# Performance work log

Measured on AMD Instinct MI355X. Metric: run time of the kernel, lower is better.

## Reference

```python
import jax, jax.numpy as jnp
import numpy as np

D_MODEL = 1024
N_HEADS = 16
D_HEAD = D_MODEL // N_HEADS


def setup_inputs() -> dict:
    key = jax.random.key(0)
    ks = jax.random.split(key, 5)
    scale = 1.0 / np.sqrt(D_MODEL)
    return {
        "x": jax.random.normal(ks[0], (2, 2048, D_MODEL), dtype=jnp.float32),
        "W_q": jax.random.normal(ks[1], (D_MODEL, D_MODEL), dtype=jnp.float32) * scale,
        "W_k": jax.random.normal(ks[2], (D_MODEL, D_MODEL), dtype=jnp.float32) * scale,
        "W_v": jax.random.normal(ks[3], (D_MODEL, D_MODEL), dtype=jnp.float32) * scale,
        "W_o": jax.random.normal(ks[4], (D_MODEL, D_MODEL), dtype=jnp.float32) * scale,
    }


def reference(x, W_q, W_k, W_v, W_o):
    B, S, _ = x.shape
    # nn.Linear computes x @ W.T; weights stored [out, in]
    def proj(W):
        y = jnp.einsum("bsd,ed->bse", x, W)
        return y.reshape(B, S, N_HEADS, D_HEAD).transpose(0, 2, 1, 3)  # [B,H,S,Dh]

    q, k, v = proj(W_q), proj(W_k), proj(W_v)
    scores = jnp.einsum("bhqd,bhkd->bhqk", q, k) / jnp.sqrt(jnp.float32(D_HEAD))
    causal = jnp.triu(jnp.ones((S, S), dtype=bool), k=1)
    scores = jnp.where(causal, -jnp.inf, scores)
    attn = jax.nn.softmax(scores, axis=-1)
    out = jnp.einsum("bhqk,bhkd->bhqd", attn, v)  # [B,H,S,Dh]
    out = out.transpose(0, 2, 1, 3).reshape(B, S, D_MODEL)
    return jnp.einsum("bsd,ed->bse", out, W_o)
```

## Files before the change

kernel.cpp:

```cpp
#include <hip/hip_runtime.h>


#define DMODEL 1024
#define NHEADS 16
#define DHEAD  64
#define SEQ    2048
#define BATCH  2
#define MROWS  (BATCH * SEQ)

typedef __bf16 bf16x8 __attribute__((ext_vector_type(8)));
typedef __bf16 bf16x4 __attribute__((ext_vector_type(4)));
typedef float  f32x4  __attribute__((ext_vector_type(4)));

__device__ __forceinline__ f32x4 mfma16(bf16x8 a, bf16x8 b, f32x4 c) {
    return __builtin_amdgcn_mfma_f32_16x16x32_bf16(a, b, c, 0, 0, 0);
}

__device__ __forceinline__ bf16x8 ld8(const float* p) {
    const f32x4 a0 = *(const f32x4*)p;
    const f32x4 a1 = *(const f32x4*)(p + 4);
    bf16x8 v;
    v[0] = (__bf16)a0[0]; v[1] = (__bf16)a0[1];
    v[2] = (__bf16)a0[2]; v[3] = (__bf16)a0[3];
    v[4] = (__bf16)a1[0]; v[5] = (__bf16)a1[1];
    v[6] = (__bf16)a1[2]; v[7] = (__bf16)a1[3];
    return v;
}

__device__ __forceinline__ void gll16(const __bf16* g, __bf16* l) {
    __builtin_amdgcn_global_load_lds(
        (const __attribute__((address_space(1))) void*)g,
        (__attribute__((address_space(3))) void*)l,
        16, 0, 0);
}

__global__ __launch_bounds__(256) void cvt_kernel(const float* __restrict__ x,
                                                  const float* __restrict__ Wq,
                                                  const float* __restrict__ Wk,
                                                  const float* __restrict__ Wv,
                                                  const float* __restrict__ Wo,
                                                  __bf16* __restrict__ xb,
                                                  __bf16* __restrict__ wcat) {
    const int y = blockIdx.y;
    const float* src;
    __bf16* dst;
    int nchunks;
    if (y == 0) { src = x; dst = xb; nchunks = (MROWS * DMODEL) / 8; }
    else {
        src = (y == 1) ? Wq : (y == 2) ? Wk : (y == 3) ? Wv : Wo;
        dst = wcat + (size_t)(y - 1) * DMODEL * DMODEL;
        nchunks = (DMODEL * DMODEL) / 8;
    }
    const int c = blockIdx.x * 256 + threadIdx.x;
    if (c < nchunks) *(bf16x8*)(dst + (size_t)c * 8) = ld8(src + (size_t)c * 8);
}

template <typename TC>
__device__ __forceinline__ void gemm_bb_body(const __bf16* __restrict__ A,
                                             const __bf16* __restrict__ W,
                                             TC* __restrict__ C,
                                             int m0, int n0, float scale) {
    constexpr int K = DMODEL;
    __shared__ __align__(16) __bf16 As[128][32];
    __shared__ __align__(16) __bf16 Bs[128][32];

    const int tid  = threadIdx.x;
    const int lane = tid & 63;
    const int wave = tid >> 6;
    const int quad = lane >> 4;
    const int l16  = lane & 15;
    const int wm   = wave & 1;
    const int wn   = wave >> 1;

    const int srow = lane >> 2;
    const int scol = (lane & 3) * 8;

    const __bf16* a0p = A + (size_t)(m0 + wave * 16 + srow) * K + scol;
    const __bf16* a1p = A + (size_t)(m0 + 64 + wave * 16 + srow) * K + scol;
    const __bf16* b0p = W + (size_t)(n0 + wave * 16 + srow) * K + scol;
    const __bf16* b1p = W + (size_t)(n0 + 64 + wave * 16 + srow) * K + scol;

    f32x4 acc[4][4] = {};

    for (int k0 = 0; k0 < K; k0 += 32) {
        __syncthreads();
        gll16(a0p + k0, &As[wave * 16][0]);
        gll16(a1p + k0, &As[64 + wave * 16][0]);
        gll16(b0p + k0, &Bs[wave * 16][0]);
        gll16(b1p + k0, &Bs[64 + wave * 16][0]);
        __syncthreads();

        bf16x8 af[4], bfr[4];
#pragma unroll
        for (int i = 0; i < 4; ++i) {
            af[i]  = *(const bf16x8*)(&As[wm * 64 + i * 16 + l16][quad * 8]);
            bfr[i] = *(const bf16x8*)(&Bs[wn * 64 + i * 16 + l16][quad * 8]);
        }
#pragma unroll
        for (int mi = 0; mi < 4; ++mi)
#pragma unroll
            for (int ni = 0; ni < 4; ++ni)
                acc[mi][ni] = mfma16(af[mi], bfr[ni], acc[mi][ni]);
    }

#pragma unroll
    for (int mi = 0; mi < 4; ++mi)
#pragma unroll
        for (int ni = 0; ni < 4; ++ni)
#pragma unroll
            for (int r = 0; r < 4; ++r) {
                int row = m0 + wm * 64 + mi * 16 + quad * 4 + r;
                int col = n0 + wn * 64 + ni * 16 + l16;
                C[(size_t)row * DMODEL + col] = (TC)(acc[mi][ni][r] * scale);
            }
}

#define QSCALE 0.1803368801111204f

__global__ __launch_bounds__(256) void qkv_kernel(const __bf16* __restrict__ X,
                                                  const __bf16* __restrict__ wcat,
                                                  __bf16* __restrict__ QKV) {
    const __bf16* W = wcat + (size_t)blockIdx.z * DMODEL * DMODEL;
    __bf16*       Y = QKV + (size_t)blockIdx.z * MROWS * DMODEL;
    const float scale = (blockIdx.z == 0) ? QSCALE : 1.0f;
    gemm_bb_body<__bf16>(X, W, Y, blockIdx.y * 128, blockIdx.x * 128, scale);
}

__global__ __launch_bounds__(256) void out_gemm_kernel(const __bf16* __restrict__ A,
                                                       const __bf16* __restrict__ W,
                                                       float* __restrict__ C) {
    gemm_bb_body<float>(A, W, C, blockIdx.y * 128, blockIdx.x * 128, 1.0f);
}

__global__ __launch_bounds__(128) void attn_kernel(const __bf16* __restrict__ Q,
                                                   const __bf16* __restrict__ Kg,
                                                   const __bf16* __restrict__ Vg,
                                                   __bf16* __restrict__ O) {
    const int bh = blockIdx.x;
    const int qt = 63 - blockIdx.y;
    const int b = bh >> 4, h = bh & 15;
    const size_t base = (size_t)b * SEQ * DMODEL + (size_t)h * DHEAD;

    const int tid  = threadIdx.x;
    const int lane = tid & 63;
    const int wave = tid >> 6;
    const int quad = lane >> 4;
    const int l16  = lane & 15;

    __shared__ __align__(16) __bf16 Ks[32][80];
    __shared__ __align__(16) __bf16 Vt[64][40];
    __shared__ __align__(16) __bf16 Ps[2][16][40];

    const int ldr = tid >> 2;
    const int c0  = (tid & 3) * 16;
    const int vcol = (((ldr >> 3) ^ (c0 >> 4)) << 3) | (ldr & 7);

    const int qrow = qt * 32 + wave * 16 + l16;

    const bf16x8 qf0 = *(const bf16x8*)(Q + base + (size_t)qrow * DMODEL + quad * 8);
    const bf16x8 qf1 = *(const bf16x8*)(Q + base + (size_t)qrow * DMODEL + 32 + quad * 8);

    f32x4 oacc[4] = {};
    float m_i = -1e30f, l_i = 0.f;

    const __bf16* kp = Kg + base + (size_t)ldr * DMODEL + c0;
    const __bf16* vp = Vg + base + (size_t)ldr * DMODEL + c0;
    bf16x8 pk0 = *(const bf16x8*)(kp);
    bf16x8 pk1 = *(const bf16x8*)(kp + 8);
    bf16x8 pv0 = *(const bf16x8*)(vp);
    bf16x8 pv1 = *(const bf16x8*)(vp + 8);

    for (int kt = 0; kt <= qt; ++kt) {
        *(bf16x8*)(&Ks[ldr][c0])     = pk0;
        *(bf16x8*)(&Ks[ldr][c0 + 8]) = pk1;
#pragma unroll
        for (int i = 0; i < 8; ++i) {
            Vt[c0 + i][vcol]     = pv0[i];
            Vt[c0 + 8 + i][vcol] = pv1[i];
        }
        __syncthreads();

        if (kt < qt) {
            const __bf16* kp2 = Kg + base + (size_t)((kt + 1) * 32 + ldr) * DMODEL + c0;
            const __bf16* vp2 = Vg + base + (size_t)((kt + 1) * 32 + ldr) * DMODEL + c0;
            pk0 = *(const bf16x8*)(kp2);
            pk1 = *(const bf16x8*)(kp2 + 8);
            pv0 = *(const bf16x8*)(vp2);
            pv1 = *(const bf16x8*)(vp2 + 8);
        }

        const int k0 = kt * 32;
        const bool diag = (kt == qt);

        const bf16x8 kf00 = *(const bf16x8*)(&Ks[l16][quad * 8]);
        const bf16x8 kf01 = *(const bf16x8*)(&Ks[l16][32 + quad * 8]);
        const bf16x8 kf10 = *(const bf16x8*)(&Ks[16 + l16][quad * 8]);
        const bf16x8 kf11 = *(const bf16x8*)(&Ks[16 + l16][32 + quad * 8]);
        f32x4 s0 = {}, s1 = {};
        s0 = mfma16(kf00, qf0, s0); s0 = mfma16(kf01, qf1, s0);
        s1 = mfma16(kf10, qf0, s1); s1 = mfma16(kf11, qf1, s1);

        float mx;
        bool ok[2][4];
        if (!diag) {
            float m0 = s0[0];
#pragma unroll
            for (int r = 1; r < 4; ++r) m0 = fmaxf(m0, s0[r]);
#pragma unroll
            for (int r = 0; r < 4; ++r) m0 = fmaxf(m0, s1[r]);
            mx = m0;
        } else {
            mx = -1e30f;
#pragma unroll
            for (int hh = 0; hh < 2; ++hh)
#pragma unroll
                for (int r = 0; r < 4; ++r) {
                    const int kk = k0 + hh * 16 + quad * 4 + r;
                    ok[hh][r] = (kk <= qrow);
                    const float v = hh ? s1[r] : s0[r];
                    mx = fmaxf(mx, ok[hh][r] ? v : -1e30f);
                }
        }
        mx = fmaxf(mx, __shfl_xor(mx, 16));
        mx = fmaxf(mx, __shfl_xor(mx, 32));
        const float mnew  = fmaxf(m_i, mx);
        const float alpha = exp2f(m_i - mnew);
        m_i = mnew;

        float p[2][4];
        float rs = 0.f;
        if (!diag) {
#pragma unroll
            for (int hh = 0; hh < 2; ++hh)
#pragma unroll
                for (int r = 0; r < 4; ++r) {
                    p[hh][r] = exp2f((hh ? s1[r] : s0[r]) - mnew);
                    rs += p[hh][r];
                }
        } else {
#pragma unroll
            for (int hh = 0; hh < 2; ++hh)
#pragma unroll
                for (int r = 0; r < 4; ++r) {
                    p[hh][r] = ok[hh][r] ? exp2f((hh ? s1[r] : s0[r]) - mnew) : 0.f;
                    rs += p[hh][r];
                }
        }
        rs += __shfl_xor(rs, 16);
        rs += __shfl_xor(rs, 32);
        l_i = l_i * alpha + rs;

        bf16x4 w0, w1;
#pragma unroll
        for (int r = 0; r < 4; ++r) { w0[r] = (__bf16)p[0][r]; w1[r] = (__bf16)p[1][r]; }
        *(bf16x4*)(&Ps[wave][l16][quad * 4])      = w0;
        *(bf16x4*)(&Ps[wave][l16][16 + quad * 4]) = w1;

        const bf16x8 pf = *(const bf16x8*)(&Ps[wave][l16][quad * 8]);
#pragma unroll
        for (int f = 0; f < 4; ++f) {
            const bf16x8 vf = *(const bf16x8*)(&Vt[f * 16 + l16][(quad ^ f) * 8]);
            oacc[f] = mfma16(vf, pf, oacc[f] * alpha);
        }
        __syncthreads();
    }

    const float inv = (l_i > 0.f) ? (1.f / l_i) : 0.f;
#pragma unroll
    for (int f = 0; f < 4; ++f) {
        bf16x4 o;
#pragma unroll
        for (int r = 0; r < 4; ++r) o[r] = (__bf16)(oacc[f][r] * inv);
        *(bf16x4*)(O + base + (size_t)qrow * DMODEL + f * 16 + quad * 4) = o;
    }
}

extern "C" void kernel_launch(void* const* d_in, const int* in_sizes, int n_in,
                              void* d_out, int out_size, void* d_ws, size_t ws_size,
                              hipStream_t stream) {
    const float* x  = (const float*)d_in[0];
    const float* Wq = (const float*)d_in[1];
    const float* Wk = (const float*)d_in[2];
    const float* Wv = (const float*)d_in[3];
    const float* Wo = (const float*)d_in[4];
    float* out = (float*)d_out;

    const size_t tm = (size_t)MROWS * DMODEL;
    const size_t tw = (size_t)DMODEL * DMODEL;
    __bf16* QKV  = (__bf16*)d_ws;
    __bf16* xb   = QKV + 3 * tm;
    __bf16* wcat = xb + tm;
    __bf16* Q = QKV;
    __bf16* K = QKV + tm;
    __bf16* V = QKV + 2 * tm;

    dim3 gc(2048, 5);
    cvt_kernel<<<gc, 256, 0, stream>>>(x, Wq, Wk, Wv, Wo, xb, wcat);

    dim3 g1(DMODEL / 128, MROWS / 128, 3);
    qkv_kernel<<<g1, 256, 0, stream>>>(xb, wcat, QKV);

    dim3 g2(BATCH * NHEADS, SEQ / 32);
    attn_kernel<<<g2, 128, 0, stream>>>(Q, K, V, Q);

    dim3 g3(DMODEL / 128, MROWS / 128);
    out_gemm_kernel<<<g3, 256, 0, stream>>>(Q, wcat + 3 * tw, out);
}
```

Baseline: 203.2 us.

## Write V transposed from QKV GEMM and load attention tiles via direct-to-LDS loads

The QKV GEMM now writes V in a transposed [head_dim, tokens] layout, and its K step doubles to 64 with an XOR-swizzled LDS layout. The attention kernel stages K and V^T tiles with direct global-to-LDS loads instead of register prefetch plus a scalar transpose scatter into shared memory. This removes the per-element V transpose in attention and the padded LDS arrays. In exchange it drops the register prefetch overlap and the trailing barrier, and the transposed V store from the GEMM is narrow and strided.

Result: slower. 217.5 us (+7.0%).

```diff
diff --git a/kernel.cpp b/kernel.cpp
--- a/kernel.cpp
+++ b/kernel.cpp
@@ -59,10 +59,12 @@
 __device__ __forceinline__ void gemm_bb_body(const __bf16* __restrict__ A,
                                              const __bf16* __restrict__ W,
                                              TC* __restrict__ C,
-                                             int m0, int n0, float scale) {
+                                             __bf16* __restrict__ VT,
+                                             bool vt, int m0, int n0,
+                                             float scale) {
     constexpr int K = DMODEL;
-    __shared__ __align__(16) __bf16 As[128][32];
-    __shared__ __align__(16) __bf16 Bs[128][32];
+    __shared__ __align__(16) __bf16 As[128][64];
+    __shared__ __align__(16) __bf16 Bs[128][64];
 
     const int tid  = threadIdx.x;
     const int lane = tid & 63;
@@ -72,69 +74,89 @@
     const int wm   = wave & 1;
     const int wn   = wave >> 1;
 
-    const int srow = lane >> 2;
-    const int scol = (lane & 3) * 8;
-
-    const __bf16* a0p = A + (size_t)(m0 + wave * 16 + srow) * K + scol;
-    const __bf16* a1p = A + (size_t)(m0 + 64 + wave * 16 + srow) * K + scol;
-    const __bf16* b0p = W + (size_t)(n0 + wave * 16 + srow) * K + scol;
-    const __bf16* b1p = W + (size_t)(n0 + 64 + wave * 16 + srow) * K + scol;
+    const int sr = lane >> 3;
+    const int sc = ((lane & 7) ^ sr) * 8;
 
     f32x4 acc[4][4] = {};
 
-    for (int k0 = 0; k0 < K; k0 += 32) {
+    for (int k0 = 0; k0 < K; k0 += 64) {
         __syncthreads();
-        gll16(a0p + k0, &As[wave * 16][0]);
-        gll16(a1p + k0, &As[64 + wave * 16][0]);
-        gll16(b0p + k0, &Bs[wave * 16][0]);
-        gll16(b1p + k0, &Bs[64 + wave * 16][0]);
+#pragma unroll
+        for (int s = 0; s < 4; ++s) {
+            const int row = s * 32 + wave * 8 + sr;
+            gll16(A + (size_t)(m0 + row) * K + k0 + sc, &As[s * 32 + wave * 8][0]);
+            gll16(W + (size_t)(n0 + row) * K + k0 + sc, &Bs[s * 32 + wave * 8][0]);
+        }
         __syncthreads();
 
-        bf16x8 af[4], bfr[4];
-#pragma unroll
-        for (int i = 0; i < 4; ++i) {
-            af[i]  = *(const bf16x8*)(&As[wm * 64 + i * 16 + l16][quad * 8]);
-            bfr[i] = *(const bf16x8*)(&Bs[wn * 64 + i * 16 + l16][quad * 8]);
-        }
+#pragma unroll
+        for (int h = 0; h < 2; ++h) {
+            bf16x8 af[4], bfr[4];
+#pragma unroll
+            for (int i = 0; i < 4; ++i) {
+                const int gr = ((h * 4 + quad) ^ (l16 & 7)) * 8;
+                af[i]  = *(const bf16x8*)(&As[wm * 64 + i * 16 + l16][gr]);
+                bfr[i] = *(const bf16x8*)(&Bs[wn * 64 + i * 16 + l16][gr]);
+            }
+#pragma unroll
+            for (int mi = 0; mi < 4; ++mi)
+#pragma unroll
+                for (int ni = 0; ni < 4; ++ni)
+                    acc[mi][ni] = mfma16(af[mi], bfr[ni], acc[mi][ni]);
+        }
+    }
+
+    if (!vt) {
 #pragma unroll
         for (int mi = 0; mi < 4; ++mi)
 #pragma unroll
             for (int ni = 0; ni < 4; ++ni)
-                acc[mi][ni] = mfma16(af[mi], bfr[ni], acc[mi][ni]);
-    }
-
-#pragma unroll
-    for (int mi = 0; mi < 4; ++mi)
-#pragma unroll
-        for (int ni = 0; ni < 4; ++ni)
-#pragma unroll
-            for (int r = 0; r < 4; ++r) {
-                int row = m0 + wm * 64 + mi * 16 + quad * 4 + r;
-                int col = n0 + wn * 64 + ni * 16 + l16;
-                C[(size_t)row * DMODEL + col] = (TC)(acc[mi][ni][r] * scale);
+#pragma unroll
+                for (int r = 0; r < 4; ++r) {
+                    int row = m0 + wm * 64 + mi * 16 + quad * 4 + r;
+                    int col = n0 + wn * 64 + ni * 16 + l16;
+                    C[(size_t)row * DMODEL + col] = (TC)(acc[mi][ni][r] * scale);
+                }
+    } else {
+#pragma unroll
+        for (int mi = 0; mi < 4; ++mi)
+#pragma unroll
+            for (int ni = 0; ni < 4; ++ni) {
+                const int m  = m0 + wm * 64 + mi * 16 + quad * 4;
+                const int hd = n0 + wn * 64 + ni * 16 + l16;
+                bf16x4 v4;
+#pragma unroll
+                for (int r = 0; r < 4; ++r) v4[r] = (__bf16)acc[mi][ni][r];
+                *(bf16x4*)(VT + (size_t)hd * MROWS + m) = v4;
             }
+    }
 }
 
 #define QSCALE 0.1803368801111204f
 
 __global__ __launch_bounds__(256) void qkv_kernel(const __bf16* __restrict__ X,
                                                   const __bf16* __restrict__ wcat,
-                                                  __bf16* __restrict__ QKV) {
-    const __bf16* W = wcat + (size_t)blockIdx.z * DMODEL * DMODEL;
-    __bf16*       Y = QKV + (size_t)blockIdx.z * MROWS * DMODEL;
-    const float scale = (blockIdx.z == 0) ? QSCALE : 1.0f;
-    gemm_bb_body<__bf16>(X, W, Y, blockIdx.y * 128, blockIdx.x * 128, scale);
+                                                  __bf16* __restrict__ Q,
+                                                  __bf16* __restrict__ K,
+                                                  __bf16* __restrict__ VT) {
+    const int z = blockIdx.z;
+    const __bf16* W = wcat + (size_t)z * DMODEL * DMODEL;
+    __bf16* Y = (z == 0) ? Q : K;
+    const float scale = (z == 0) ? QSCALE : 1.0f;
+    gemm_bb_body<__bf16>(X, W, Y, VT, z == 2,
+                         blockIdx.y * 128, blockIdx.x * 128, scale);
 }
 
 __global__ __launch_bounds__(256) void out_gemm_kernel(const __bf16* __restrict__ A,
                                                        const __bf16* __restrict__ W,
                                                        float* __restrict__ C) {
-    gemm_bb_body<float>(A, W, C, blockIdx.y * 128, blockIdx.x * 128, 1.0f);
+    gemm_bb_body<float>(A, W, C, nullptr, false,
+                        blockIdx.y * 128, blockIdx.x * 128, 1.0f);
 }
 
 __global__ __launch_bounds__(128) void attn_kernel(const __bf16* __restrict__ Q,
                                                    const __bf16* __restrict__ Kg,
-                                                   const __bf16* __restrict__ Vg,
+                                                   const __bf16* __restrict__ VTg,
                                                    __bf16* __restrict__ O) {
     const int bh = blockIdx.x;
     const int qt = 63 - blockIdx.y;
@@ -147,13 +169,14 @@
     const int quad = lane >> 4;
     const int l16  = lane & 15;
 
-    __shared__ __align__(16) __bf16 Ks[32][80];
-    __shared__ __align__(16) __bf16 Vt[64][40];
+    __shared__ __align__(16) __bf16 Ks[32][64];
+    __shared__ __align__(16) __bf16 Vs[64][32];
     __shared__ __align__(16) __bf16 Ps[2][16][40];
 
-    const int ldr = tid >> 2;
-    const int c0  = (tid & 3) * 16;
-    const int vcol = (((ldr >> 3) ^ (c0 >> 4)) << 3) | (ldr & 7);
+    const int ksr = lane >> 3;
+    const int ksc = ((lane & 7) ^ ksr) * 8;
+    const int vsr = lane >> 2;
+    const int vsc = ((lane & 3) ^ ((lane >> 3) & 3)) * 8;
 
     const int qrow = qt * 32 + wave * 16 + l16;
 
@@ -163,39 +186,27 @@
     f32x4 oacc[4] = {};
     float m_i = -1e30f, l_i = 0.f;
 
-    const __bf16* kp = Kg + base + (size_t)ldr * DMODEL + c0;
-    const __bf16* vp = Vg + base + (size_t)ldr * DMODEL + c0;
-    bf16x8 pk0 = *(const bf16x8*)(kp);
-    bf16x8 pk1 = *(const bf16x8*)(kp + 8);
-    bf16x8 pv0 = *(const bf16x8*)(vp);
-    bf16x8 pv1 = *(const bf16x8*)(vp + 8);
-
     for (int kt = 0; kt <= qt; ++kt) {
-        *(bf16x8*)(&Ks[ldr][c0])     = pk0;
-        *(bf16x8*)(&Ks[ldr][c0 + 8]) = pk1;
-#pragma unroll
-        for (int i = 0; i < 8; ++i) {
-            Vt[c0 + i][vcol]     = pv0[i];
-            Vt[c0 + 8 + i][vcol] = pv1[i];
-        }
+        const int k0 = kt * 32;
         __syncthreads();
-
-        if (kt < qt) {
-            const __bf16* kp2 = Kg + base + (size_t)((kt + 1) * 32 + ldr) * DMODEL + c0;
-            const __bf16* vp2 = Vg + base + (size_t)((kt + 1) * 32 + ldr) * DMODEL + c0;
-            pk0 = *(const bf16x8*)(kp2);
-            pk1 = *(const bf16x8*)(kp2 + 8);
-            pv0 = *(const bf16x8*)(vp2);
-            pv1 = *(const bf16x8*)(vp2 + 8);
-        }
-
-        const int k0 = kt * 32;
+#pragma unroll
+        for (int j = 0; j < 2; ++j) {
+            gll16(Kg + base + (size_t)(k0 + wave * 16 + j * 8 + ksr) * DMODEL + ksc,
+                  &Ks[wave * 16 + j * 8][0]);
+            gll16(VTg + (size_t)(h * 64 + j * 32 + wave * 16 + vsr) * MROWS
+                      + (size_t)b * SEQ + k0 + vsc,
+                  &Vs[j * 32 + wave * 16][0]);
+        }
+        __syncthreads();
+
         const bool diag = (kt == qt);
 
-        const bf16x8 kf00 = *(const bf16x8*)(&Ks[l16][quad * 8]);
-        const bf16x8 kf01 = *(const bf16x8*)(&Ks[l16][32 + quad * 8]);
-        const bf16x8 kf10 = *(const bf16x8*)(&Ks[16 + l16][quad * 8]);
-        const bf16x8 kf11 = *(const bf16x8*)(&Ks[16 + l16][32 + quad * 8]);
+        const int g0 = ((quad ^ (l16 & 7))) * 8;
+        const int g1 = ((quad ^ 4) ^ (l16 & 7)) * 8;
+        const bf16x8 kf00 = *(const bf16x8*)(&Ks[l16][g0]);
+        const bf16x8 kf01 = *(const bf16x8*)(&Ks[l16][g1]);
+        const bf16x8 kf10 = *(const bf16x8*)(&Ks[16 + l16][g0]);
+        const bf16x8 kf11 = *(const bf16x8*)(&Ks[16 + l16][g1]);
         f32x4 s0 = {}, s1 = {};
         s0 = mfma16(kf00, qf0, s0); s0 = mfma16(kf01, qf1, s0);
         s1 = mfma16(kf10, qf0, s1); s1 = mfma16(kf11, qf1, s1);
@@ -257,12 +268,12 @@
         *(bf16x4*)(&Ps[wave][l16][16 + quad * 4]) = w1;
 
         const bf16x8 pf = *(const bf16x8*)(&Ps[wave][l16][quad * 8]);
+        const int vg = (quad ^ ((l16 >> 1) & 3)) * 8;
 #pragma unroll
         for (int f = 0; f < 4; ++f) {
-            const bf16x8 vf = *(const bf16x8*)(&Vt[f * 16 + l16][(quad ^ f) * 8]);
+            const bf16x8 vf = *(const bf16x8*)(&Vs[f * 16 + l16][vg]);
             oacc[f] = mfma16(vf, pf, oacc[f] * alpha);
         }
-        __syncthreads();
     }
 
     const float inv = (l_i > 0.f) ? (1.f / l_i) : 0.f;
@@ -287,21 +298,20 @@
 
     const size_t tm = (size_t)MROWS * DMODEL;
     const size_t tw = (size_t)DMODEL * DMODEL;
-    __bf16* QKV  = (__bf16*)d_ws;
-    __bf16* xb   = QKV + 3 * tm;
+    __bf16* Q    = (__bf16*)d_ws;
+    __bf16* K    = Q + tm;
+    __bf16* VT   = K + tm;
+    __bf16* xb   = VT + tm;
     __bf16* wcat = xb + tm;
-    __bf16* Q = QKV;
-    __bf16* K = QKV + tm;
-    __bf16* V = QKV + 2 * tm;
 
     dim3 gc(2048, 5);
     cvt_kernel<<<gc, 256, 0, stream>>>(x, Wq, Wk, Wv, Wo, xb, wcat);
 
     dim3 g1(DMODEL / 128, MROWS / 128, 3);
-    qkv_kernel<<<g1, 256, 0, stream>>>(xb, wcat, QKV);
+    qkv_kernel<<<g1, 256, 0, stream>>>(xb, wcat, Q, K, VT);
 
     dim3 g2(BATCH * NHEADS, SEQ / 32);
-    attn_kernel<<<g2, 128, 0, stream>>>(Q, K, V, Q);
+    attn_kernel<<<g2, 128, 0, stream>>>(Q, K, VT, Q);
 
     dim3 g3(DMODEL / 128, MROWS / 128);
     out_gemm_kernel<<<g3, 256, 0, stream>>>(Q, wcat + 3 * tw, out);
```
